# Kernel optimization log

Measured on AMD Instinct MI355X. Metric: run time of the kernel, lower is better.

The kernel has to match this reference:

```python
import jax, jax.numpy as jnp
import numpy as np

# Fixed production-scale dims (equal-size graphs -> no ragged padding needed)
B, NPG, C, H, L, FFN, NC = 16, 512, 128, 8, 4, 512, 4
D = C // H          # head dim = 16
T = NPG + 1         # +1 virtual graph token
EPG = 8192          # edges per graph (avg degree 16)
E = B * EPG


def _ln(x, g, b, eps=1e-5):
    m = x.mean(-1, keepdims=True)
    v = ((x - m) ** 2).mean(-1, keepdims=True)
    return (x - m) * jax.lax.rsqrt(v + eps) * g + b


def setup_inputs() -> dict:
    key = jax.random.key(0)
    ks = jax.random.split(key, 24)
    N = B * NPG
    node_feats = jax.random.normal(ks[0], (N, 3), jnp.float32)
    # intra-graph edges: local endpoints + per-graph node offset (matches batch_ptr math)
    local = jax.random.randint(ks[1], (2, B, EPG), 0, NPG)
    offs = (jnp.arange(B) * NPG)[None, :, None]
    edge_index = (local + offs).reshape(2, E)
    edge_attr = jax.random.randint(ks[2], (E,), 0, 10)

    def nrm(k, shape, scale=0.02):
        return jax.random.normal(k, shape, jnp.float32) * scale

    params = {
        "W_node": nrm(ks[3], (3, C), 0.3), "b_node": jnp.zeros((C,), jnp.float32),
        "graph_token": nrm(ks[4], (C,), 1.0),
        "edge_bias_table": nrm(ks[5], (11, H), 0.1).at[0].set(0.0),  # padding_idx=0
        "in_deg_emb": nrm(ks[6], (512, C)).at[0].set(0.0),           # padding_idx=0
        "out_deg_emb": nrm(ks[7], (512, C)).at[0].set(0.0),
        "vnode_bias": nrm(ks[8], (H,), 1.0),
        "Wq": nrm(ks[9], (L, C, C)), "bq": jnp.zeros((L, C), jnp.float32),
        "Wk": nrm(ks[10], (L, C, C)), "bk": jnp.zeros((L, C), jnp.float32),
        "Wv": nrm(ks[11], (L, C, C)), "bv": jnp.zeros((L, C), jnp.float32),
        "Wo": nrm(ks[12], (L, C, C)), "bo": jnp.zeros((L, C), jnp.float32),
        "ln1_g": jnp.ones((L, C), jnp.float32), "ln1_b": jnp.zeros((L, C), jnp.float32),
        "ln2_g": jnp.ones((L, C), jnp.float32), "ln2_b": jnp.zeros((L, C), jnp.float32),
        "W1": nrm(ks[13], (L, C, FFN)), "b1": jnp.zeros((L, FFN), jnp.float32),
        "W2": nrm(ks[14], (L, FFN, C)), "b2": jnp.zeros((L, C), jnp.float32),
        "normf_g": jnp.ones((C,), jnp.float32), "normf_b": jnp.zeros((C,), jnp.float32),
        "Wc1": nrm(ks[15], (C, C // 2)), "bc1": jnp.zeros((C // 2,), jnp.float32),
        "Wc2": nrm(ks[16], (C // 2, NC)), "bc2": jnp.zeros((NC,), jnp.float32),
    }
    return {"node_feats": node_feats, "edge_index": edge_index,
            "edge_attr": edge_attr, "num_graphs": B, **params}


def reference(node_feats, W_node, b_node, graph_token, edge_bias_table,
              in_deg_emb, out_deg_emb, vnode_bias,
              Wq, bq, Wk, bk, Wv, bv, Wo, bo,
              ln1_g, ln1_b, ln2_g, ln2_b, W1, b1, W2, b2,
              normf_g, normf_b, Wc1, bc1, Wc2, bc2,
              edge_index, edge_attr, num_graphs):
    N = node_feats.shape[0]
    npg = N // num_graphs
    t = npg + 1
    src, dst = edge_index[0], edge_index[1]
    # degree encoders (scatter_add of ones == segment_sum)
    in_deg = jnp.clip(jax.ops.segment_sum(jnp.ones_like(dst), dst, num_segments=N), 0, 511)
    out_deg = jnp.clip(jax.ops.segment_sum(jnp.ones_like(src), src, num_segments=N), 0, 511)
    x_enc = node_feats @ W_node + b_node + in_deg_emb[in_deg] + out_deg_emb[out_deg]
    # equal-size graphs with sorted batch ids -> padding loop is a reshape, mask all-False
    x = jnp.concatenate(
        [jnp.broadcast_to(graph_token, (num_graphs, 1, C)),
         x_enc.reshape(num_graphs, npg, C)], axis=1)  # [B, T, C]
    # attention bias: vnode row/col + scattered edge-attr embeddings
    bias = jnp.zeros((num_graphs, H, t, t), jnp.float32)
    bias = bias.at[:, :, 0, :].set(vnode_bias[None, :, None])
    bias = bias.at[:, :, :, 0].set(vnode_bias[None, :, None])
    eb = edge_bias_table[jnp.clip(edge_attr, 0, 9) + 1]  # [E, H]
    g = src // npg
    sl = src - g * npg + 1
    dl = dst - g * npg + 1
    bias = bias.at[g, :, sl, dl].add(eb)  # duplicate edges accumulate (scatter_add)
    scale = 1.0 / np.sqrt(D).astype(np.float32)
    for l in range(L):  # key_padding_mask is all-False here -> masked_fill is a no-op
        h = _ln(x, ln1_g[l], ln1_b[l])
        q = (h @ Wq[l] + bq[l]).reshape(num_graphs, t, H, D)
        k = (h @ Wk[l] + bk[l]).reshape(num_graphs, t, H, D)
        v = (h @ Wv[l] + bv[l]).reshape(num_graphs, t, H, D)
        scores = jnp.einsum('bthd,bshd->bhts', q, k) * scale + bias
        attn = jax.nn.softmax(scores, axis=-1)
        o = jnp.einsum('bhts,bshd->bthd', attn, v).reshape(num_graphs, t, C)
        x = x + o @ Wo[l] + bo[l]
        h2 = _ln(x, ln2_g[l], ln2_b[l])
        x = x + jax.nn.gelu(h2 @ W1[l] + b1[l], approximate=False) @ W2[l] + b2[l]
    x = _ln(x, normf_g, normf_b)
    gr = x[:, 0, :]  # virtual-node readout
    return jax.nn.gelu(gr @ Wc1 + bc1, approximate=False) @ Wc2 + bc2
```

## Files before the change

### kernel.cpp

```cpp
#include <hip/hip_runtime.h>
#include <hip/hip_bf16.h>

#define BB 16
#define NPG 512
#define CC 128
#define HH 8
#define LL 4
#define FFN 512
#define NCLS 4
#define DD 16
#define TT 513
#define EE 131072
#define NNODES 8192
#define ROWS (BB * TT)
#define ECAP 64
#define SP 544
#define BSTR 292

static constexpr size_t XROWS = (size_t)BB * TT;
static constexpr size_t XSZ   = XROWS * CC;
static constexpr size_t VTSZ  = (size_t)BB * HH * DD * SP;

typedef unsigned short ushort_t;
typedef __attribute__((ext_vector_type(8))) short short8;
typedef __attribute__((ext_vector_type(4))) float floatx4;

__device__ __forceinline__ float gelu_exact(float v) {
    return 0.5f * v * (1.0f + erff(v * 0.70710678118654752440f));
}
__device__ __forceinline__ ushort_t f2bf(float f) {
    union { float f; unsigned u; } c; c.f = f;
    unsigned u = c.u;
    return (ushort_t)((u + 0x7FFFu + ((u >> 16) & 1u)) >> 16);
}
__device__ __forceinline__ int swz(int row, int col, int stride) {
    int kb = col >> 3;
    return row * stride + (((kb ^ (row & 7)) << 3) | (col & 7));
}

__global__ __launch_bounds__(256) void deg_csr_kernel(const int* __restrict__ ei,
                                                      const int* __restrict__ ea,
                                                      int* __restrict__ deg_in,
                                                      int* __restrict__ deg_out,
                                                      int* __restrict__ cnt,
                                                      int* __restrict__ ebuf) {
    int e = blockIdx.x * 256 + threadIdx.x;
    if (e >= EE) return;
    int src = ei[e], dst = ei[EE + e];
    atomicAdd(&deg_out[src], 1);
    atomicAdd(&deg_in[dst], 1);
    int g = src >> 9;
    int sl = src - (g << 9) + 1;
    int dl = dst - (g << 9) + 1;
    int a = ea[e];
    a = (a < 0) ? 0 : (a > 9 ? 9 : a);
    a += 1;
    int row = g * TT + sl;
    int pos = atomicAdd(&cnt[row], 1);
    if (pos < ECAP) ebuf[(size_t)row * ECAP + pos] = dl | (a << 16);
}

__global__ __launch_bounds__(256) void encode_kernel(const float* __restrict__ nf,
                                                     const float* __restrict__ Wn,
                                                     const float* __restrict__ bn,
                                                     const float* __restrict__ gt,
                                                     const float* __restrict__ ide,
                                                     const float* __restrict__ ode,
                                                     const int* __restrict__ deg_in,
                                                     const int* __restrict__ deg_out,
                                                     float* __restrict__ x) {
    int gid = blockIdx.x * 256 + threadIdx.x;
    if (gid >= (int)(XROWS * CC)) return;
    int c = gid & (CC - 1);
    int row = gid >> 7;
    int b = row / TT;
    int t = row - b * TT;
    float val;
    if (t == 0) {
        val = gt[c];
    } else {
        int i = b * NPG + t - 1;
        val = bn[c] + nf[i*3+0]*Wn[0*CC + c] + nf[i*3+1]*Wn[1*CC + c] + nf[i*3+2]*Wn[2*CC + c];
        int di = min(deg_in[i], 511);
        int dq = min(deg_out[i], 511);
        val += ide[(size_t)di * CC + c] + ode[(size_t)dq * CC + c];
    }
    x[(size_t)row * CC + c] = val;
}

struct TrDesc {
    const float* src[24];
    ushort_t*    dst[24];
    int          K[24];
    int          N[24];
};
__global__ __launch_bounds__(256) void tr_kernel(TrDesc d) {
    int z = blockIdx.z;
    int K = d.K[z], N = d.N[z];
    int tilesN = N >> 6;
    int ntile = (K >> 6) * tilesN;
    int tile = blockIdx.x;
    if (tile >= ntile) return;
    int k0 = (tile / tilesN) << 6;
    int n0 = (tile - (tile / tilesN) * tilesN) << 6;
    const float* src = d.src[z];
    ushort_t* dst = d.dst[z];
    __shared__ float t[64][65];
    int tid = threadIdx.x;
    int c = tid & 63, rb = tid >> 6;
    #pragma unroll
    for (int kk = 0; kk < 64; kk += 4)
        t[kk + rb][c] = src[(size_t)(k0 + kk + rb) * N + n0 + c];
    __syncthreads();
    #pragma unroll
    for (int nn = 0; nn < 64; nn += 4)
        dst[(size_t)(n0 + nn + rb) * K + k0 + c] = f2bf(t[c][nn + rb]);
}

__global__ __launch_bounds__(256) void ln_kernel(const float* __restrict__ in,
                                                 ushort_t* __restrict__ out,
                                                 const float* __restrict__ gg,
                                                 const float* __restrict__ bb) {
    int tid = threadIdx.x;
    int r2 = tid >> 7;
    int c = tid & 127;
    int row = blockIdx.x * 2 + r2;
    float v = in[(size_t)row * CC + c];
    float s1 = v, s2 = v * v;
    #pragma unroll
    for (int m = 32; m >= 1; m >>= 1) {
        s1 += __shfl_xor(s1, m, 64);
        s2 += __shfl_xor(s2, m, 64);
    }
    __shared__ float red[8];
    int w = tid >> 6;
    if ((tid & 63) == 0) { red[w*2] = s1; red[w*2+1] = s2; }
    __syncthreads();
    int wb = r2 * 4;
    float S1 = red[wb] + red[wb+2], S2 = red[wb+1] + red[wb+3];
    float mn = S1 * (1.0f/CC);
    float var = S2 * (1.0f/CC) - mn * mn;
    float rs = rsqrtf(var + 1e-5f);
    out[(size_t)row * CC + c] = f2bf((v - mn) * rs * gg[c] + bb[c]);
}

struct GP {
    const ushort_t* Wt[3];
    const float*    bias[3];
    ushort_t*       outB[3];
    float           scl[3];
    int             md[3];
};
template<int K>
__global__ __launch_bounds__(256) void gemm_wave(const ushort_t* __restrict__ A, GP p,
                                                 int M, int N,
                                                 int mtiles, int ntiles) {
    int z = blockIdx.z;
    int wave = threadIdx.x >> 6;
    int wid = blockIdx.x * 4 + wave;
    int maxw = mtiles * ntiles;
    if (wid >= maxw) return;
    int tm = wid / ntiles, tn = wid - tm * ntiles;
    int m0 = tm * 16, n0 = tn * 32;
    int lane = threadIdx.x & 63, lq = lane & 15, quad = lane >> 4;
    const short* Wt = (const short*)p.Wt[z];
    const short* Ab = (const short*)A;

    size_t rowA  = (size_t)(m0 + lq) * K;
    size_t rowB0 = (size_t)(n0 + lq) * K;
    size_t rowB1 = (size_t)(n0 + 16 + lq) * K;

    floatx4 acc0 = {0.f, 0.f, 0.f, 0.f}, acc1 = acc0;
    #pragma unroll 4
    for (int k0 = 0; k0 < K; k0 += 32) {
        short8 af = *(const short8*)(Ab + rowA + k0 + quad * 8);
        short8 b0 = *(const short8*)(Wt + rowB0 + k0 + quad * 8);
        short8 b1 = *(const short8*)(Wt + rowB1 + k0 + quad * 8);
        acc0 = __builtin_amdgcn_mfma_f32_16x16x32_bf16(af, b0, acc0, 0, 0, 0);
        acc1 = __builtin_amdgcn_mfma_f32_16x16x32_bf16(af, b1, acc1, 0, 0, 0);
    }

    int mode = p.md[z];
    float scl = p.scl[z];
    ushort_t* outB = p.outB[z];
    int c0 = n0 + lq, c1 = n0 + 16 + lq;
    float bv0 = p.bias[z][c0], bv1 = p.bias[z][c1];

    #pragma unroll
    for (int rg = 0; rg < 4; ++rg) {
        int r = m0 + quad * 4 + rg;
        float a0 = acc0[rg] + bv0;
        float a1 = acc1[rg] + bv1;
        if (mode == 0) {
            outB[(size_t)r * N + c0] = f2bf(a0 * scl);
            outB[(size_t)r * N + c1] = f2bf(a1 * scl);
        } else {
            int bq = r / TT;
            int s = r - bq * TT;
            outB[((size_t)(bq * HH + (c0 >> 4)) * DD + (c0 & 15)) * SP + s] = f2bf(a0);
            outB[((size_t)(bq * HH + (c1 >> 4)) * DD + (c1 & 15)) * SP + s] = f2bf(a1);
        }
    }
}

__global__ __launch_bounds__(256) void mega_kernel(const ushort_t* __restrict__ obf,
                                                   const ushort_t* __restrict__ WtO,
                                                   const float* __restrict__ bo_,
                                                   const float* __restrict__ ln2g_,
                                                   const float* __restrict__ ln2b_,
                                                   const ushort_t* __restrict__ Wt1_,
                                                   const float* __restrict__ b1_,
                                                   const ushort_t* __restrict__ Wt2_,
                                                   const float* __restrict__ b2_,
                                                   const float* __restrict__ ln1g_,
                                                   const float* __restrict__ ln1b_,
                                                   float* __restrict__ x_,
                                                   ushort_t* __restrict__ hbf_) {
    int m0 = blockIdx.x * 16;
    int tid = threadIdx.x;
    int wave = tid >> 6, lane = tid & 63, lq = lane & 15, quad = lane >> 4;

    __shared__ ushort_t hs[16 * 128];
    __shared__ ushort_t ms[16 * 512];
    __shared__ float sred[4][16][2];

    int n0 = wave * 32;
    int c0 = n0 + lq, c1 = n0 + 16 + lq;
    float vv0[4], vv1[4];

    {
        const short* Ab = (const short*)obf;
        const short* W = (const short*)WtO;
        size_t rowA = (size_t)(m0 + lq) * CC;
        size_t rB0 = (size_t)(n0 + lq) * CC, rB1 = (size_t)(n0 + 16 + lq) * CC;
        floatx4 a0 = {0.f,0.f,0.f,0.f}, a1 = a0;
        #pragma unroll
        for (int k0 = 0; k0 < CC; k0 += 32) {
            short8 af = *(const short8*)(Ab + rowA + k0 + quad * 8);
            short8 b0 = *(const short8*)(W + rB0 + k0 + quad * 8);
            short8 b1 = *(const short8*)(W + rB1 + k0 + quad * 8);
            a0 = __builtin_amdgcn_mfma_f32_16x16x32_bf16(af, b0, a0, 0, 0, 0);
            a1 = __builtin_amdgcn_mfma_f32_16x16x32_bf16(af, b1, a1, 0, 0, 0);
        }
        float bv0 = bo_[c0], bv1 = bo_[c1];
        #pragma unroll
        for (int rg = 0; rg < 4; ++rg) {
            int r = m0 + quad * 4 + rg;
            vv0[rg] = a0[rg] + bv0 + x_[(size_t)r * CC + c0];
            vv1[rg] = a1[rg] + bv1 + x_[(size_t)r * CC + c1];
        }
        #pragma unroll
        for (int rg = 0; rg < 4; ++rg) {
            float s1 = vv0[rg] + vv1[rg];
            float s2 = vv0[rg]*vv0[rg] + vv1[rg]*vv1[rg];
            #pragma unroll
            for (int m = 1; m < 16; m <<= 1) {
                s1 += __shfl_xor(s1, m, 64);
                s2 += __shfl_xor(s2, m, 64);
            }
            if (lq == 0) { sred[wave][quad*4+rg][0] = s1; sred[wave][quad*4+rg][1] = s2; }
        }
        __syncthreads();
        float g0 = ln2g_[c0], g1 = ln2g_[c1], lb0 = ln2b_[c0], lb1 = ln2b_[c1];
        #pragma unroll
        for (int rg = 0; rg < 4; ++rg) {
            int row = quad * 4 + rg;
            float S1 = sred[0][row][0] + sred[1][row][0] + sred[2][row][0] + sred[3][row][0];
            float S2 = sred[0][row][1] + sred[1][row][1] + sred[2][row][1] + sred[3][row][1];
            float mn = S1 * (1.0f/CC);
            float var = S2 * (1.0f/CC) - mn * mn;
            float rs = rsqrtf(var + 1e-5f);
            hs[swz(row, c0, 128)] = f2bf((vv0[rg] - mn) * rs * g0 + lb0);
            hs[swz(row, c1, 128)] = f2bf((vv1[rg] - mn) * rs * g1 + lb1);
        }
    }
    __syncthreads();

    {
        const short* hsS = (const short*)hs;
        const short* W = (const short*)Wt1_;
        #pragma unroll
        for (int nt = 0; nt < 4; ++nt) {
            int n = wave * 128 + nt * 32;
            size_t rB0 = (size_t)(n + lq) * CC, rB1 = (size_t)(n + 16 + lq) * CC;
            floatx4 a0 = {0.f,0.f,0.f,0.f}, a1 = a0;
            #pragma unroll
            for (int k0 = 0; k0 < CC; k0 += 32) {
                short8 af = *(const short8*)(hsS + swz(lq, k0 + quad * 8, 128));
                short8 b0 = *(const short8*)(W + rB0 + k0 + quad * 8);
                short8 b1 = *(const short8*)(W + rB1 + k0 + quad * 8);
                a0 = __builtin_amdgcn_mfma_f32_16x16x32_bf16(af, b0, a0, 0, 0, 0);
                a1 = __builtin_amdgcn_mfma_f32_16x16x32_bf16(af, b1, a1, 0, 0, 0);
            }
            float bb0 = b1_[n + lq], bb1 = b1_[n + 16 + lq];
            #pragma unroll
            for (int rg = 0; rg < 4; ++rg) {
                int row = quad * 4 + rg;
                ms[swz(row, n + lq, 512)]      = f2bf(gelu_exact(a0[rg] + bb0));
                ms[swz(row, n + 16 + lq, 512)] = f2bf(gelu_exact(a1[rg] + bb1));
            }
        }
    }
    __syncthreads();

    {
        const short* msS = (const short*)ms;
        const short* W = (const short*)Wt2_;
        size_t rB0 = (size_t)(n0 + lq) * FFN, rB1 = (size_t)(n0 + 16 + lq) * FFN;
        floatx4 a0 = {0.f,0.f,0.f,0.f}, a1 = a0;
        #pragma unroll 4
        for (int k0 = 0; k0 < FFN; k0 += 32) {
            short8 af = *(const short8*)(msS + swz(lq, k0 + quad * 8, 512));
            short8 b0 = *(const short8*)(W + rB0 + k0 + quad * 8);
            short8 b1 = *(const short8*)(W + rB1 + k0 + quad * 8);
            a0 = __builtin_amdgcn_mfma_f32_16x16x32_bf16(af, b0, a0, 0, 0, 0);
            a1 = __builtin_amdgcn_mfma_f32_16x16x32_bf16(af, b1, a1, 0, 0, 0);
        }
        float bv0 = b2_[c0], bv1 = b2_[c1];
        float w0[4], w1[4];
        #pragma unroll
        for (int rg = 0; rg < 4; ++rg) {
            int r = m0 + quad * 4 + rg;
            w0[rg] = a0[rg] + bv0 + vv0[rg];
            w1[rg] = a1[rg] + bv1 + vv1[rg];
            x_[(size_t)r * CC + c0] = w0[rg];
            x_[(size_t)r * CC + c1] = w1[rg];
        }
        #pragma unroll
        for (int rg = 0; rg < 4; ++rg) {
            float s1 = w0[rg] + w1[rg];
            float s2 = w0[rg]*w0[rg] + w1[rg]*w1[rg];
            #pragma unroll
            for (int m = 1; m < 16; m <<= 1) {
                s1 += __shfl_xor(s1, m, 64);
                s2 += __shfl_xor(s2, m, 64);
            }
            if (lq == 0) { sred[wave][quad*4+rg][0] = s1; sred[wave][quad*4+rg][1] = s2; }
        }
        __syncthreads();
        float g0 = ln1g_[c0], g1 = ln1g_[c1], lb0 = ln1b_[c0], lb1 = ln1b_[c1];
        #pragma unroll
        for (int rg = 0; rg < 4; ++rg) {
            int row = quad * 4 + rg;
            float S1 = sred[0][row][0] + sred[1][row][0] + sred[2][row][0] + sred[3][row][0];
            float S2 = sred[0][row][1] + sred[1][row][1] + sred[2][row][1] + sred[3][row][1];
            float mn = S1 * (1.0f/CC);
            float var = S2 * (1.0f/CC) - mn * mn;
            float rs = rsqrtf(var + 1e-5f);
            int r = m0 + row;
            hbf_[(size_t)r * CC + c0] = f2bf((w0[rg] - mn) * rs * g0 + lb0);
            hbf_[(size_t)r * CC + c1] = f2bf((w1[rg] - mn) * rs * g1 + lb1);
        }
    }
}

__global__ __launch_bounds__(256) void attn_kernel(const ushort_t* __restrict__ qb,
                                                   const ushort_t* __restrict__ kb,
                                                   const ushort_t* __restrict__ vt,
                                                   const int* __restrict__ cnt,
                                                   const int* __restrict__ ebuf,
                                                   const float* __restrict__ ebt,
                                                   const float* __restrict__ vnode,
                                                   ushort_t* __restrict__ ob) {
    int bh = blockIdx.x;
    int qt = blockIdx.y;
    int b = bh >> 3, h = bh & (HH - 1);
    int tid = threadIdx.x;
    int wave = tid >> 6, lane = tid & 63, lq = lane & 15, quad = lane >> 4;

    __shared__ float arena[16 * BSTR];
    float* bstrip = arena;

    int qg = qt * 16 + lq;
    int qr = qg < TT ? qg : TT - 1;
    short8 qf = {0,0,0,0,0,0,0,0};
    if (quad < 2)
        qf = *(const short8*)(qb + ((size_t)(b * TT + qr)) * CC + h * DD + quad * 8);
    float vbh = vnode[h];
    int ql = tid >> 4, e0 = tid & 15;
    int qs = qt * 16 + ql;
    int crow = b * TT + (qs < TT ? qs : 0);
    int cn = (qs > 0 && qs < TT) ? min(cnt[crow], ECAP) : 0;

    const short* kbS = (const short*)kb;
    const short* vtS = (const short*)(vt + (size_t)bh * DD * SP);

    floatx4 oacc = {0.f, 0.f, 0.f, 0.f};
    float lsum = 0.f;

    #pragma unroll
    for (int ch = 0; ch < 2; ++ch) {
        int sp_lo = ch ? 9 : 0;
        int sp_hi = ch ? 17 : 9;
        int s_lo  = ch ? 288 : 0;
        int nrows = ch ? 256 : 288;

        int sp = sp_lo + wave;
        short8 af0 = {0,0,0,0,0,0,0,0}, af1 = af0, vf = af0;
        if (sp < sp_hi) {
            int st0 = sp * 2, st1 = sp * 2 + 1;
            int kr0 = min(b * TT + st0 * 16 + lq, (int)XROWS - 1);
            int kr1 = min(b * TT + st1 * 16 + lq, (int)XROWS - 1);
            if (quad < 2) {
                af0 = *(const short8*)(kbS + (size_t)kr0 * CC + h * DD + quad * 8);
                af1 = *(const short8*)(kbS + (size_t)kr1 * CC + h * DD + quad * 8);
            }
            vf = *(const short8*)(vtS + (size_t)lq * SP + sp * 32 + quad * 8);
        }

        for (int i = tid; i < 16 * BSTR / 4; i += 256)
            ((float4*)bstrip)[i] = make_float4(0.f, 0.f, 0.f, 0.f);
        __syncthreads();
        if (ch == 0 && tid < 16) {
            int q = qt * 16 + tid;
            if (q > 0 && q < TT) bstrip[tid * BSTR] = vbh;
        }
        for (int j = e0; j < cn; j += 16) {
            int e = ebuf[(size_t)crow * ECAP + j];
            int dl = e & 0xFFFF, a = e >> 16;
            int loc = dl - s_lo;
            if (loc >= 0 && loc < nrows)
                atomicAdd(&bstrip[ql * BSTR + loc], ebt[a * 8 + h]);
        }
        __syncthreads();

        for (; sp < sp_hi; sp += 4) {
            int spn = sp + 4;
            short8 nf0 = {0,0,0,0,0,0,0,0}, nf1 = nf0, nvf = nf0;
            if (spn < sp_hi) {
                int st0 = spn * 2, st1 = spn * 2 + 1;
                int kr0 = min(b * TT + st0 * 16 + lq, (int)XROWS - 1);
                int kr1 = min(b * TT + st1 * 16 + lq, (int)XROWS - 1);
                if (quad < 2) {
                    nf0 = *(const short8*)(kbS + (size_t)kr0 * CC + h * DD + quad * 8);
                    nf1 = *(const short8*)(kbS + (size_t)kr1 * CC + h * DD + quad * 8);
                }
                nvf = *(const short8*)(vtS + (size_t)lq * SP + spn * 32 + quad * 8);
            }

            unsigned pw[2][2];
            #pragma unroll
            for (int t = 0; t < 2; ++t) {
                int st = sp * 2 + t;
                floatx4 c = __builtin_amdgcn_mfma_f32_16x16x32_bf16(
                    t ? af1 : af0, qf, (floatx4){0.f, 0.f, 0.f, 0.f}, 0, 0, 0);
                float4 bi = *(const float4*)(bstrip + lq * BSTR + (st * 16 - s_lo) + quad * 4);
                float biv[4] = {bi.x, bi.y, bi.z, bi.w};
                float pr[4];
                #pragma unroll
                for (int rg = 0; rg < 4; ++rg) {
                    int s = st * 16 + quad * 4 + rg;
                    float p = 0.f;
                    if (s < TT) p = __expf(c[rg] + biv[rg]);
                    lsum += p;
                    pr[rg] = p;
                }
                pw[t][0] = (unsigned)f2bf(pr[0]) | ((unsigned)f2bf(pr[1]) << 16);
                pw[t][1] = (unsigned)f2bf(pr[2]) | ((unsigned)f2bf(pr[3]) << 16);
            }
            int srcA = lq + (((2 * quad) & 3) << 4);
            int srcB = lq + (((2 * quad + 1) & 3) << 4);
            int a00 = __shfl((int)pw[0][0], srcA, 64);
            int a01 = __shfl((int)pw[0][1], srcA, 64);
            int a10 = __shfl((int)pw[1][0], srcA, 64);
            int a11 = __shfl((int)pw[1][1], srcA, 64);
            int b00 = __shfl((int)pw[0][0], srcB, 64);
            int b01 = __shfl((int)pw[0][1], srcB, 64);
            int b10 = __shfl((int)pw[1][0], srcB, 64);
            int b11 = __shfl((int)pw[1][1], srcB, 64);
            union { int u[4]; short8 s8; } pu;
            bool lo = quad < 2;
            pu.u[0] = lo ? a00 : a10;
            pu.u[1] = lo ? a01 : a11;
            pu.u[2] = lo ? b00 : b10;
            pu.u[3] = lo ? b01 : b11;
            oacc = __builtin_amdgcn_mfma_f32_16x16x32_bf16(vf, pu.s8, oacc, 0, 0, 0);

            af0 = nf0; af1 = nf1; vf = nvf;
        }
        __syncthreads();
    }

    lsum += __shfl_xor(lsum, 16, 64);
    lsum += __shfl_xor(lsum, 32, 64);
    float* redw = arena;
    float* lsumS = arena + 1088;
    #pragma unroll
    for (int rg = 0; rg < 4; ++rg)
        redw[wave * 272 + (quad * 4 + rg) * 17 + lq] = oacc[rg];
    if (quad == 0) lsumS[wave * 16 + lq] = lsum;
    __syncthreads();

    {
        int q = tid >> 4, d = tid & 15;
        float o = 0.f, L = 0.f;
        #pragma unroll
        for (int w = 0; w < 4; ++w) {
            o += redw[w * 272 + d * 17 + q];
            L += lsumS[w * 16 + q];
        }
        int qq = qt * 16 + q;
        if (qq < TT)
            ob[((size_t)(b * TT + qq)) * CC + h * DD + d] = f2bf(o / L);
    }
}

__global__ __launch_bounds__(128) void head_kernel(const float* __restrict__ x,
                                                   const float* __restrict__ ng,
                                                   const float* __restrict__ nb,
                                                   const float* __restrict__ Wc1,
                                                   const float* __restrict__ bc1,
                                                   const float* __restrict__ Wc2,
                                                   const float* __restrict__ bc2,
                                                   float* __restrict__ out) {
    int b = blockIdx.x;
    int c = threadIdx.x;
    __shared__ float xfs[CC];
    __shared__ float c1s[64];
    __shared__ float red[4];

    float v = x[((size_t)b * TT) * CC + c];
    float s1 = v, s2 = v * v;
    #pragma unroll
    for (int m = 32; m >= 1; m >>= 1) {
        s1 += __shfl_xor(s1, m, 64);
        s2 += __shfl_xor(s2, m, 64);
    }
    int w = c >> 6;
    if ((c & 63) == 0) { red[w*2] = s1; red[w*2+1] = s2; }
    __syncthreads();
    float S1 = red[0] + red[2], S2 = red[1] + red[3];
    float mn = S1 * (1.0f/CC);
    float var = S2 * (1.0f/CC) - mn * mn;
    float rs = rsqrtf(var + 1e-5f);
    xfs[c] = (v - mn) * rs * ng[c] + nb[c];
    __syncthreads();
    if (c < 64) {
        float a = bc1[c];
        #pragma unroll 4
        for (int k = 0; k < CC; ++k) a = fmaf(xfs[k], Wc1[(size_t)k * 64 + c], a);
        c1s[c] = gelu_exact(a);
    }
    __syncthreads();
    if (c < NCLS) {
        float a = bc2[c];
        #pragma unroll 4
        for (int j = 0; j < 64; ++j) a = fmaf(c1s[j], Wc2[(size_t)j * NCLS + c], a);
        out[(size_t)b * NCLS + c] = a;
    }
}

extern "C" void kernel_launch(void* const* d_in, const int* in_sizes, int n_in,
                              void* d_out, int out_size, void* d_ws, size_t ws_size,
                              hipStream_t stream) {
    const float* node_feats = (const float*)d_in[0];
    const int*   edge_index = (const int*)d_in[1];
    const int*   edge_attr  = (const int*)d_in[2];
    const float* W_node  = (const float*)d_in[4];
    const float* b_node  = (const float*)d_in[5];
    const float* g_token = (const float*)d_in[6];
    const float* ebt     = (const float*)d_in[7];
    const float* ide     = (const float*)d_in[8];
    const float* ode     = (const float*)d_in[9];
    const float* vnode   = (const float*)d_in[10];
    const float* Wq = (const float*)d_in[11];
    const float* bq = (const float*)d_in[12];
    const float* Wk = (const float*)d_in[13];
    const float* bk = (const float*)d_in[14];
    const float* Wv = (const float*)d_in[15];
    const float* bv = (const float*)d_in[16];
    const float* Wo = (const float*)d_in[17];
    const float* bo = (const float*)d_in[18];
    const float* ln1g = (const float*)d_in[19];
    const float* ln1b = (const float*)d_in[20];
    const float* ln2g = (const float*)d_in[21];
    const float* ln2b = (const float*)d_in[22];
    const float* W1 = (const float*)d_in[23];
    const float* b1 = (const float*)d_in[24];
    const float* W2 = (const float*)d_in[25];
    const float* b2 = (const float*)d_in[26];
    const float* nfg = (const float*)d_in[27];
    const float* nfb = (const float*)d_in[28];
    const float* Wc1 = (const float*)d_in[29];
    const float* bc1 = (const float*)d_in[30];
    const float* Wc2 = (const float*)d_in[31];
    const float* bc2 = (const float*)d_in[32];
    float* out = (float*)d_out;

    char* base = (char*)d_ws;
    float* x      = (float*)base;     base += XSZ * 4;
    ushort_t* hbf = (ushort_t*)base;  base += XSZ * 2;
    ushort_t* qb  = (ushort_t*)base;  base += XSZ * 2;
    ushort_t* kb  = (ushort_t*)base;  base += XSZ * 2;
    ushort_t* vt  = (ushort_t*)base;  base += VTSZ * 2;
    ushort_t* obf = (ushort_t*)base;  base += XSZ * 2;
    ushort_t* wtqkvo = (ushort_t*)base; base += (size_t)16 * 16384 * 2;
    ushort_t* wt1 = (ushort_t*)base;  base += (size_t)4 * 65536 * 2;
    ushort_t* wt2 = (ushort_t*)base;  base += (size_t)4 * 65536 * 2;
    int* deg_in  = (int*)base;        base += NNODES * 4;
    int* deg_out = (int*)base;        base += NNODES * 4;
    int* cnt     = (int*)base;        base += (size_t)ROWS * 4;
    int* ebuf    = (int*)base;        base += (size_t)ROWS * ECAP * 4;

    hipMemsetAsync(deg_in, 0, (size_t)(2 * NNODES + ROWS) * 4, stream);
    deg_csr_kernel<<<EE / 256, 256, 0, stream>>>(edge_index, edge_attr,
                                                 deg_in, deg_out, cnt, ebuf);
    encode_kernel<<<(int)((XROWS * CC + 255) / 256), 256, 0, stream>>>(
        node_feats, W_node, b_node, g_token, ide, ode, deg_in, deg_out, x);

    TrDesc td;
    for (int l = 0; l < LL; ++l) {
        const float* srcs[4] = {Wq + (size_t)l*CC*CC, Wk + (size_t)l*CC*CC,
                                Wv + (size_t)l*CC*CC, Wo + (size_t)l*CC*CC};
        for (int k = 0; k < 4; ++k) {
            int slot = k * 4 + l;
            td.src[slot] = srcs[k];
            td.dst[slot] = wtqkvo + (size_t)slot * 16384;
            td.K[slot] = CC; td.N[slot] = CC;
        }
        td.src[16 + l] = W1 + (size_t)l*CC*FFN;
        td.dst[16 + l] = wt1 + (size_t)l*65536;
        td.K[16 + l] = CC; td.N[16 + l] = FFN;
        td.src[20 + l] = W2 + (size_t)l*FFN*CC;
        td.dst[20 + l] = wt2 + (size_t)l*65536;
        td.K[20 + l] = FFN; td.N[20 + l] = CC;
    }
    tr_kernel<<<dim3(16, 1, 24), 256, 0, stream>>>(td);

    const int MT16 = (int)(XROWS / 16);

    ln_kernel<<<(int)(XROWS / 2), 256, 0, stream>>>(x, hbf, ln1g, ln1b);

    for (int l = 0; l < LL; ++l) {
        GP pq = {};
        pq.Wt[0] = wtqkvo + (size_t)(0*4+l)*16384;
        pq.Wt[1] = wtqkvo + (size_t)(1*4+l)*16384;
        pq.Wt[2] = wtqkvo + (size_t)(2*4+l)*16384;
        pq.bias[0] = bq + l*CC; pq.bias[1] = bk + l*CC; pq.bias[2] = bv + l*CC;
        pq.outB[0] = qb; pq.outB[1] = kb; pq.outB[2] = vt;
        pq.scl[0] = 0.25f; pq.scl[1] = 1.0f; pq.scl[2] = 1.0f;
        pq.md[0] = 0; pq.md[1] = 0; pq.md[2] = 3;
        gemm_wave<CC><<<dim3(MT16, 1, 3), 256, 0, stream>>>(
            hbf, pq, (int)XROWS, CC, MT16, 4);

        attn_kernel<<<dim3(BB*HH, 33), 256, 0, stream>>>(
            qb, kb, vt, cnt, ebuf, ebt, vnode, obf);

        int ln_next = (l + 1) % LL;
        mega_kernel<<<MT16, 256, 0, stream>>>(
            obf,
            wtqkvo + (size_t)(3*4+l)*16384, bo + l*CC,
            ln2g + l*CC, ln2b + l*CC,
            wt1 + (size_t)l*65536, b1 + l*FFN,
            wt2 + (size_t)l*65536, b2 + l*CC,
            ln1g + ln_next*CC, ln1b + ln_next*CC,
            x, hbf);
    }

    head_kernel<<<BB, 128, 0, stream>>>(x, nfg, nfb, Wc1, bc1, Wc2, bc2, out);
}
```

Before: 452.2 us.

## Fuse LN1 and QKV projection into the mega kernel and a pre-kernel

Removes the standalone QKV GEMM launch and the bf16 LN1 output buffer. The next layer's LayerNorm result now stays in shared memory inside mega_kernel, and each block computes Q, K and V for its own 16 rows. A new pre_kernel does the same for layer 0, and the last layer skips the QKV stage. This saves launches and a global round-trip of the normalized activations, at the cost of longer per-block serial work in mega_kernel and a triple GEMM per wave.

```diff
diff --git a/kernel.cpp b/kernel.cpp
--- a/kernel.cpp
+++ b/kernel.cpp
@@ -36,6 +36,53 @@
 __device__ __forceinline__ int swz(int row, int col, int stride) {
     int kb = col >> 3;
     return row * stride + (((kb ^ (row & 7)) << 3) | (col & 7));
+}
+
+__device__ __forceinline__ void qkv_stage(const ushort_t* hs,
+                                          const ushort_t* Wtq, const float* bq_,
+                                          const ushort_t* Wtk, const float* bk_,
+                                          const ushort_t* Wtv, const float* bv_,
+                                          ushort_t* qb, ushort_t* kb, ushort_t* vt,
+                                          int m0, int wave, int lq, int quad) {
+    const short* hsS = (const short*)hs;
+    int n0 = wave * 32;
+    int c0 = n0 + lq, c1 = n0 + 16 + lq;
+    const short* Ws[3] = {(const short*)Wtq, (const short*)Wtk, (const short*)Wtv};
+    const float* bs[3] = {bq_, bk_, bv_};
+    size_t rB0 = (size_t)(n0 + lq) * CC, rB1 = (size_t)(n0 + 16 + lq) * CC;
+
+    #pragma unroll
+    for (int m = 0; m < 3; ++m) {
+        const short* W = Ws[m];
+        floatx4 a0 = {0.f,0.f,0.f,0.f}, a1 = a0;
+        #pragma unroll
+        for (int k0 = 0; k0 < CC; k0 += 32) {
+            short8 af = *(const short8*)(hsS + swz(lq, k0 + quad * 8, 128));
+            short8 b0 = *(const short8*)(W + rB0 + k0 + quad * 8);
+            short8 b1 = *(const short8*)(W + rB1 + k0 + quad * 8);
+            a0 = __builtin_amdgcn_mfma_f32_16x16x32_bf16(af, b0, a0, 0, 0, 0);
+            a1 = __builtin_amdgcn_mfma_f32_16x16x32_bf16(af, b1, a1, 0, 0, 0);
+        }
+        float bv0 = bs[m][c0], bv1 = bs[m][c1];
+        #pragma unroll
+        for (int rg = 0; rg < 4; ++rg) {
+            int r = m0 + quad * 4 + rg;
+            float v0 = a0[rg] + bv0;
+            float v1 = a1[rg] + bv1;
+            if (m == 0) {
+                qb[(size_t)r * CC + c0] = f2bf(v0 * 0.25f);
+                qb[(size_t)r * CC + c1] = f2bf(v1 * 0.25f);
+            } else if (m == 1) {
+                kb[(size_t)r * CC + c0] = f2bf(v0);
+                kb[(size_t)r * CC + c1] = f2bf(v1);
+            } else {
+                int bg = r / TT;
+                int s = r - bg * TT;
+                vt[((size_t)(bg * HH + (c0 >> 4)) * DD + (c0 & 15)) * SP + s] = f2bf(v0);
+                vt[((size_t)(bg * HH + (c1 >> 4)) * DD + (c1 & 15)) * SP + s] = f2bf(v1);
+            }
+        }
+    }
 }
 
 __global__ __launch_bounds__(256) void deg_csr_kernel(const int* __restrict__ ei,
@@ -117,90 +164,60 @@
         dst[(size_t)(n0 + nn + rb) * K + k0 + c] = f2bf(t[c][nn + rb]);
 }
 
-__global__ __launch_bounds__(256) void ln_kernel(const float* __restrict__ in,
-                                                 ushort_t* __restrict__ out,
-                                                 const float* __restrict__ gg,
-                                                 const float* __restrict__ bb) {
+__global__ __launch_bounds__(256) void pre_kernel(const float* __restrict__ x_,
+                                                  const float* __restrict__ ln1g_,
+                                                  const float* __restrict__ ln1b_,
+                                                  const ushort_t* __restrict__ Wtq,
+                                                  const float* __restrict__ bq_,
+                                                  const ushort_t* __restrict__ Wtk,
+                                                  const float* __restrict__ bk_,
+                                                  const ushort_t* __restrict__ Wtv,
+                                                  const float* __restrict__ bv_,
+                                                  ushort_t* __restrict__ qb,
+                                                  ushort_t* __restrict__ kb,
+                                                  ushort_t* __restrict__ vt) {
+    int m0 = blockIdx.x * 16;
     int tid = threadIdx.x;
-    int r2 = tid >> 7;
-    int c = tid & 127;
-    int row = blockIdx.x * 2 + r2;
-    float v = in[(size_t)row * CC + c];
-    float s1 = v, s2 = v * v;
-    #pragma unroll
-    for (int m = 32; m >= 1; m >>= 1) {
-        s1 += __shfl_xor(s1, m, 64);
-        s2 += __shfl_xor(s2, m, 64);
-    }
-    __shared__ float red[8];
-    int w = tid >> 6;
-    if ((tid & 63) == 0) { red[w*2] = s1; red[w*2+1] = s2; }
-    __syncthreads();
-    int wb = r2 * 4;
-    float S1 = red[wb] + red[wb+2], S2 = red[wb+1] + red[wb+3];
-    float mn = S1 * (1.0f/CC);
-    float var = S2 * (1.0f/CC) - mn * mn;
-    float rs = rsqrtf(var + 1e-5f);
-    out[(size_t)row * CC + c] = f2bf((v - mn) * rs * gg[c] + bb[c]);
-}
-
-struct GP {
-    const ushort_t* Wt[3];
-    const float*    bias[3];
-    ushort_t*       outB[3];
-    float           scl[3];
-    int             md[3];
-};
-template<int K>
-__global__ __launch_bounds__(256) void gemm_wave(const ushort_t* __restrict__ A, GP p,
-                                                 int M, int N,
-                                                 int mtiles, int ntiles) {
-    int z = blockIdx.z;
-    int wave = threadIdx.x >> 6;
-    int wid = blockIdx.x * 4 + wave;
-    int maxw = mtiles * ntiles;
-    if (wid >= maxw) return;
-    int tm = wid / ntiles, tn = wid - tm * ntiles;
-    int m0 = tm * 16, n0 = tn * 32;
-    int lane = threadIdx.x & 63, lq = lane & 15, quad = lane >> 4;
-    const short* Wt = (const short*)p.Wt[z];
-    const short* Ab = (const short*)A;
-
-    size_t rowA  = (size_t)(m0 + lq) * K;
-    size_t rowB0 = (size_t)(n0 + lq) * K;
-    size_t rowB1 = (size_t)(n0 + 16 + lq) * K;
-
-    floatx4 acc0 = {0.f, 0.f, 0.f, 0.f}, acc1 = acc0;
-    #pragma unroll 4
-    for (int k0 = 0; k0 < K; k0 += 32) {
-        short8 af = *(const short8*)(Ab + rowA + k0 + quad * 8);
-        short8 b0 = *(const short8*)(Wt + rowB0 + k0 + quad * 8);
-        short8 b1 = *(const short8*)(Wt + rowB1 + k0 + quad * 8);
-        acc0 = __builtin_amdgcn_mfma_f32_16x16x32_bf16(af, b0, acc0, 0, 0, 0);
-        acc1 = __builtin_amdgcn_mfma_f32_16x16x32_bf16(af, b1, acc1, 0, 0, 0);
-    }
-
-    int mode = p.md[z];
-    float scl = p.scl[z];
-    ushort_t* outB = p.outB[z];
+    int wave = tid >> 6, lane = tid & 63, lq = lane & 15, quad = lane >> 4;
+
+    __shared__ ushort_t hs[16 * 128];
+    __shared__ float sred[4][16][2];
+
+    int n0 = wave * 32;
     int c0 = n0 + lq, c1 = n0 + 16 + lq;
-    float bv0 = p.bias[z][c0], bv1 = p.bias[z][c1];
-
+    float w0[4], w1[4];
     #pragma unroll
     for (int rg = 0; rg < 4; ++rg) {
         int r = m0 + quad * 4 + rg;
-        float a0 = acc0[rg] + bv0;
-        float a1 = acc1[rg] + bv1;
-        if (mode == 0) {
-            outB[(size_t)r * N + c0] = f2bf(a0 * scl);
-            outB[(size_t)r * N + c1] = f2bf(a1 * scl);
-        } else {
-            int bq = r / TT;
-            int s = r - bq * TT;
-            outB[((size_t)(bq * HH + (c0 >> 4)) * DD + (c0 & 15)) * SP + s] = f2bf(a0);
-            outB[((size_t)(bq * HH + (c1 >> 4)) * DD + (c1 & 15)) * SP + s] = f2bf(a1);
-        }
-    }
+        w0[rg] = x_[(size_t)r * CC + c0];
+        w1[rg] = x_[(size_t)r * CC + c1];
+    }
+    #pragma unroll
+    for (int rg = 0; rg < 4; ++rg) {
+        float s1 = w0[rg] + w1[rg];
+        float s2 = w0[rg]*w0[rg] + w1[rg]*w1[rg];
+        #pragma unroll
+        for (int m = 1; m < 16; m <<= 1) {
+            s1 += __shfl_xor(s1, m, 64);
+            s2 += __shfl_xor(s2, m, 64);
+        }
+        if (lq == 0) { sred[wave][quad*4+rg][0] = s1; sred[wave][quad*4+rg][1] = s2; }
+    }
+    __syncthreads();
+    float g0 = ln1g_[c0], g1 = ln1g_[c1], lb0 = ln1b_[c0], lb1 = ln1b_[c1];
+    #pragma unroll
+    for (int rg = 0; rg < 4; ++rg) {
+        int row = quad * 4 + rg;
+        float S1 = sred[0][row][0] + sred[1][row][0] + sred[2][row][0] + sred[3][row][0];
+        float S2 = sred[0][row][1] + sred[1][row][1] + sred[2][row][1] + sred[3][row][1];
+        float mn = S1 * (1.0f/CC);
+        float var = S2 * (1.0f/CC) - mn * mn;
+        float rs = rsqrtf(var + 1e-5f);
+        hs[swz(row, c0, 128)] = f2bf((w0[rg] - mn) * rs * g0 + lb0);
+        hs[swz(row, c1, 128)] = f2bf((w1[rg] - mn) * rs * g1 + lb1);
+    }
+    __syncthreads();
+    qkv_stage(hs, Wtq, bq_, Wtk, bk_, Wtv, bv_, qb, kb, vt, m0, wave, lq, quad);
 }
 
 __global__ __launch_bounds__(256) void mega_kernel(const ushort_t* __restrict__ obf,
@@ -214,8 +231,17 @@
                                                    const float* __restrict__ b2_,
                                                    const float* __restrict__ ln1g_,
                                                    const float* __restrict__ ln1b_,
+                                                   const ushort_t* __restrict__ Wtq,
+                                                   const float* __restrict__ bq_,
+                                                   const ushort_t* __restrict__ Wtk,
+                                                   const float* __restrict__ bk_,
+                                                   const ushort_t* __restrict__ Wtv,
+                                                   const float* __restrict__ bv_,
                                                    float* __restrict__ x_,
-                                                   ushort_t* __restrict__ hbf_) {
+                                                   ushort_t* __restrict__ qb,
+                                                   ushort_t* __restrict__ kb,
+                                                   ushort_t* __restrict__ vt,
+                                                   int doQKV) {
     int m0 = blockIdx.x * 16;
     int tid = threadIdx.x;
     int wave = tid >> 6, lane = tid & 63, lq = lane & 15, quad = lane >> 4;
@@ -326,6 +352,7 @@
             x_[(size_t)r * CC + c0] = w0[rg];
             x_[(size_t)r * CC + c1] = w1[rg];
         }
+        if (!doQKV) return;
         #pragma unroll
         for (int rg = 0; rg < 4; ++rg) {
             float s1 = w0[rg] + w1[rg];
@@ -347,11 +374,13 @@
             float mn = S1 * (1.0f/CC);
             float var = S2 * (1.0f/CC) - mn * mn;
             float rs = rsqrtf(var + 1e-5f);
-            int r = m0 + row;
-            hbf_[(size_t)r * CC + c0] = f2bf((w0[rg] - mn) * rs * g0 + lb0);
-            hbf_[(size_t)r * CC + c1] = f2bf((w1[rg] - mn) * rs * g1 + lb1);
-        }
-    }
+            hs[swz(row, c0, 128)] = f2bf((w0[rg] - mn) * rs * g0 + lb0);
+            hs[swz(row, c1, 128)] = f2bf((w1[rg] - mn) * rs * g1 + lb1);
+        }
+    }
+    __syncthreads();
+
+    qkv_stage(hs, Wtq, bq_, Wtk, bk_, Wtv, bv_, qb, kb, vt, m0, wave, lq, quad);
 }
 
 __global__ __launch_bounds__(256) void attn_kernel(const ushort_t* __restrict__ qb,
@@ -589,7 +618,6 @@
 
     char* base = (char*)d_ws;
     float* x      = (float*)base;     base += XSZ * 4;
-    ushort_t* hbf = (ushort_t*)base;  base += XSZ * 2;
     ushort_t* qb  = (ushort_t*)base;  base += XSZ * 2;
     ushort_t* kb  = (ushort_t*)base;  base += XSZ * 2;
     ushort_t* vt  = (ushort_t*)base;  base += VTSZ * 2;
@@ -629,32 +657,30 @@
 
     const int MT16 = (int)(XROWS / 16);
 
-    ln_kernel<<<(int)(XROWS / 2), 256, 0, stream>>>(x, hbf, ln1g, ln1b);
+    pre_kernel<<<MT16, 256, 0, stream>>>(
+        x, ln1g, ln1b,
+        wtqkvo + (size_t)(0*4+0)*16384, bq,
+        wtqkvo + (size_t)(1*4+0)*16384, bk,
+        wtqkvo + (size_t)(2*4+0)*16384, bv,
+        qb, kb, vt);
 
     for (int l = 0; l < LL; ++l) {
-        GP pq = {};
-        pq.Wt[0] = wtqkvo + (size_t)(0*4+l)*16384;
-        pq.Wt[1] = wtqkvo + (size_t)(1*4+l)*16384;
-        pq.Wt[2] = wtqkvo + (size_t)(2*4+l)*16384;
-        pq.bias[0] = bq + l*CC; pq.bias[1] = bk + l*CC; pq.bias[2] = bv + l*CC;
-        pq.outB[0] = qb; pq.outB[1] = kb; pq.outB[2] = vt;
-        pq.scl[0] = 0.25f; pq.scl[1] = 1.0f; pq.scl[2] = 1.0f;
-        pq.md[0] = 0; pq.md[1] = 0; pq.md[2] = 3;
-        gemm_wave<CC><<<dim3(MT16, 1, 3), 256, 0, stream>>>(
-            hbf, pq, (int)XROWS, CC, MT16, 4);
-
         attn_kernel<<<dim3(BB*HH, 33), 256, 0, stream>>>(
             qb, kb, vt, cnt, ebuf, ebt, vnode, obf);
 
-        int ln_next = (l + 1) % LL;
+        int ln = (l + 1) % LL;
         mega_kernel<<<MT16, 256, 0, stream>>>(
             obf,
             wtqkvo + (size_t)(3*4+l)*16384, bo + l*CC,
             ln2g + l*CC, ln2b + l*CC,
             wt1 + (size_t)l*65536, b1 + l*FFN,
             wt2 + (size_t)l*65536, b2 + l*CC,
-            ln1g + ln_next*CC, ln1b + ln_next*CC,
-            x, hbf);
+            ln1g + ln*CC, ln1b + ln*CC,
+            wtqkvo + (size_t)(0*4+ln)*16384, bq + ln*CC,
+            wtqkvo + (size_t)(1*4+ln)*16384, bk + ln*CC,
+            wtqkvo + (size_t)(2*4+ln)*16384, bv + ln*CC,
+            x, qb, kb, vt,
+            (l < LL-1) ? 1 : 0);
     }
 
     head_kernel<<<BB, 128, 0, stream>>>(x, nfg, nfb, Wc1, bc1, Wc2, bc2, out);
```

New measurement: 436.0 us. -3.6%, faster.
